# Kernel optimization log

Hardware: AMD Instinct MI355X
Metric: run time of the kernel (lower is better)

Reference implementation:

```python
import jax, jax.numpy as jnp
import numpy as np

HID = 64        # HID_DIM of seq2seq encoder
NL = 2          # N_LAYERS
D = HID * NL    # dim_hidden = 128
TYPES = 16      # node op types; Input=0, Const=1
MAX_ET = 32     # max edge_type id
NUM_ROUNDS = 2


def _gru_cell(x, h, Wih, Whh, bih, bhh):
    # torch GRU gate ordering: r, z, n
    gi = x @ Wih.T + bih
    gh = h @ Whh.T + bhh
    ir, iz, inn = jnp.split(gi, 3, axis=-1)
    hr, hz, hn = jnp.split(gh, 3, axis=-1)
    r = jax.nn.sigmoid(ir + hr)
    z = jax.nn.sigmoid(iz + hz)
    n = jnp.tanh(inn + r * hn)
    return (1.0 - z) * n + z * h


def _posenc(n, d):
    pos = jnp.arange(n, dtype=jnp.float32)[:, None]
    i = jnp.arange(d // 2, dtype=jnp.float32)[None, :]
    inv = jnp.exp(-jnp.log(10000.0) * (2.0 * i / d))
    pe = jnp.zeros((n, d), jnp.float32)
    pe = pe.at[:, 0::2].set(jnp.sin(pos * inv))
    pe = pe.at[:, 1::2].set(jnp.cos(pos * inv))
    return pe


def _forward(x, edge_index, edge_type, sim_res, seq_len,
             enc_Wih0, enc_Whh0, enc_bih0, enc_bhh0,
             enc_Wih1, enc_Whh1, enc_bih1, enc_bhh1,
             Wq, Wk, Wv, op_emb, mlp_W1, mlp_b1, mlp_W2, mlp_b2,
             gru_Wih, gru_Whh, gru_bih, gru_bhh):
    N = x.shape[0]
    # --- seq2seq encode (2-layer GRU over time), computed for all nodes then masked ---
    xs = jnp.swapaxes(sim_res[:, :seq_len, :], 0, 1)  # [T, N, W]
    h0 = jnp.zeros((N, HID), sim_res.dtype)
    h1 = jnp.zeros((N, HID), sim_res.dtype)

    def step(carry, xt):
        h0, h1 = carry
        h0 = _gru_cell(xt, h0, enc_Wih0, enc_Whh0, enc_bih0, enc_bhh0)
        h1 = _gru_cell(h0, h1, enc_Wih1, enc_Whh1, enc_bih1, enc_bhh1)
        return (h0, h1), None

    (h0, h1), _ = jax.lax.scan(step, (h0, h1), xs)
    enc = jnp.concatenate([h0, h1], axis=-1)  # [N, D] = permute(1,0,2).flatten(1)
    mask = (x[:, 0] == 1) | (x[:, 1] == 1)    # Input | Const nodes
    node_emb = jnp.where(mask[:, None], enc, 0.0)

    src, dst = edge_index[0], edge_index[1]
    edge_op = jnp.argmax(x[dst], axis=1)       # [E]
    pe = _posenc(MAX_ET, D)
    edge_feat = pe[edge_type] + op_emb[edge_op]  # [E, D]
    scale = 1.0 / jnp.sqrt(jnp.float32(D))

    for _ in range(NUM_ROUNDS):
        kf = node_emb[src] + edge_feat         # [E, D]
        q = node_emb[dst] @ Wq.T
        k = kf @ Wk.T
        v = kf @ Wv.T
        score = jnp.sum(q * k, axis=-1) * scale  # [E]
        m = jax.ops.segment_max(score, dst, num_segments=N)
        ex = jnp.exp(score - m[dst])
        den = jax.ops.segment_sum(ex, dst, num_segments=N)
        alpha = ex / (den[dst] + 1e-9)
        aggr = jax.ops.segment_sum(alpha[:, None] * v, dst, num_segments=N)  # [N, D]
        aggr = jax.nn.relu(aggr @ mlp_W1.T + mlp_b1) @ mlp_W2.T + mlp_b2
        node_emb = _gru_cell(aggr, node_emb, gru_Wih, gru_Whh, gru_bih, gru_bhh)
    return node_emb


def setup_inputs() -> dict:
    key = jax.random.key(0)
    ks = jax.random.split(key, 24)
    N, E, T, W = 20000, 320000, 32, 32
    s = 0.05

    def g(k, shape):
        return jax.random.normal(k, shape, dtype=jnp.float32) * s

    node_type = jax.random.randint(ks[0], (N,), 0, TYPES)
    x = jax.nn.one_hot(node_type, TYPES, dtype=jnp.float32)
    edge_index = jax.random.randint(ks[1], (2, E), 0, N)
    edge_type = jax.random.randint(ks[2], (E,), 0, MAX_ET)
    sim_res = jax.random.uniform(ks[3], (N, T, W), dtype=jnp.float32)
    return {
        "x": x, "edge_index": edge_index, "edge_type": edge_type,
        "sim_res": sim_res, "seq_len": 32,
        "enc_Wih0": g(ks[4], (3 * HID, W)), "enc_Whh0": g(ks[5], (3 * HID, HID)),
        "enc_bih0": g(ks[6], (3 * HID,)), "enc_bhh0": g(ks[7], (3 * HID,)),
        "enc_Wih1": g(ks[8], (3 * HID, HID)), "enc_Whh1": g(ks[9], (3 * HID, HID)),
        "enc_bih1": g(ks[10], (3 * HID,)), "enc_bhh1": g(ks[11], (3 * HID,)),
        "Wq": g(ks[12], (D, D)), "Wk": g(ks[13], (D, D)), "Wv": g(ks[14], (D, D)),
        "op_emb": g(ks[15], (TYPES, D)),
        "mlp_W1": g(ks[16], (D, D)), "mlp_b1": g(ks[17], (D,)),
        "mlp_W2": g(ks[18], (D, D)), "mlp_b2": g(ks[19], (D,)),
        "gru_Wih": g(ks[20], (3 * D, D)), "gru_Whh": g(ks[21], (3 * D, D)),
        "gru_bih": g(ks[22], (3 * D,)), "gru_bhh": g(ks[23], (3 * D,)),
    }


def reference(x, edge_index, edge_type, sim_res, seq_len,
              enc_Wih0, enc_Whh0, enc_bih0, enc_bhh0,
              enc_Wih1, enc_Whh1, enc_bih1, enc_bhh1,
              Wq, Wk, Wv, op_emb, mlp_W1, mlp_b1, mlp_W2, mlp_b2,
              gru_Wih, gru_Whh, gru_bih, gru_bhh):
    return _forward(x, edge_index, edge_type, sim_res, seq_len,
                    enc_Wih0, enc_Whh0, enc_bih0, enc_bhh0,
                    enc_Wih1, enc_Whh1, enc_bih1, enc_bhh1,
                    Wq, Wk, Wv, op_emb, mlp_W1, mlp_b1, mlp_W2, mlp_b2,
                    gru_Wih, gru_Whh, gru_bih, gru_bhh)
```

## Files before the change

### kernel.cpp

```cpp
#include <hip/hip_runtime.h>

typedef unsigned int uint;
typedef unsigned short ushort;

typedef __attribute__((ext_vector_type(8))) short bf8;
typedef __attribute__((ext_vector_type(4))) float f32x4;
typedef _Float16 half_t;
typedef __attribute__((ext_vector_type(8))) half_t h8;

__device__ __forceinline__ ushort f2bf(float f){
  uint u = __builtin_bit_cast(uint, f);
  u = u + 0x7FFFu + ((u >> 16) & 1u);
  return (ushort)(u >> 16);
}
__device__ __forceinline__ float bfl(uint u){ return __builtin_bit_cast(float, u << 16); }
__device__ __forceinline__ float bfh(uint u){ return __builtin_bit_cast(float, u & 0xFFFF0000u); }
__device__ __forceinline__ uint pkhalf(float a, float b){
  ushort lo = __builtin_bit_cast(ushort, (half_t)a);
  ushort hi = __builtin_bit_cast(ushort, (half_t)b);
  return (uint)lo | ((uint)hi << 16);
}
__device__ __forceinline__ float sigmoidf_(float x){ return 1.0f/(1.0f + __expf(-x)); }
__device__ __forceinline__ float tanhf_(float x){
  x = fminf(15.0f, fmaxf(-15.0f, x));
  float t = __expf(-2.0f*x);
  return (1.0f - t)/(1.0f + t);
}
__device__ __forceinline__ f32x4 mfma_f16(h8 a, h8 b, f32x4 c){
  return __builtin_amdgcn_mfma_f32_16x16x32_f16(a, b, c, 0, 0, 0);
}
__device__ __forceinline__ f32x4 mfma_bf(bf8 a, bf8 b, f32x4 c){
  return __builtin_amdgcn_mfma_f32_16x16x32_bf16(a, b, c, 0, 0, 0);
}
__device__ __forceinline__ h8 ldw8(const float* p){
  f32x4 a = *(const f32x4*)p, b = *(const f32x4*)(p+4);
  h8 v;
  #pragma unroll
  for (int j=0;j<4;j++){ v[j] = (half_t)a[j]; v[4+j] = (half_t)b[j]; }
  return v;
}

__global__ __launch_bounds__(256) void k_prep(const float* __restrict__ x,
    const int* __restrict__ dst,
    int* __restrict__ typ, int* __restrict__ mlist, int* __restrict__ cnt,
    int* __restrict__ deg, float* __restrict__ Hf, ushort* __restrict__ Hb,
    int N, int E){
  int i = blockIdx.x*256 + threadIdx.x;
  int total = gridDim.x*256;
  if (i < N){
    const float* xr = x + (size_t)i*16;
    int t = 0;
    #pragma unroll
    for (int j=0;j<16;j++) if (xr[j] > 0.5f) t = j;
    typ[i] = t;
    if (t < 2){
      int p = atomicAdd(cnt, 1);
      mlist[p] = i;
    }
  }
  if (i < E) atomicAdd(&deg[dst[i]], 1);
  f32x4 z4 = (f32x4)0.0f;
  for (int j = i; j < N*32; j += total) ((f32x4*)Hf)[j] = z4;
  uint2 z2; z2.x = 0u; z2.y = 0u;
  for (int j = i; j < N*32; j += total) ((uint2*)Hb)[j] = z2;
}

__global__ __launch_bounds__(256) void k_cvt(
    const float* wq, const float* wk, const float* wv,
    const float* w1, const float* w2, const float* wih, const float* whh,
    const float* __restrict__ op_emb,
    ushort* oqkv, ushort* o1, ushort* o2, ushort* oih, ushort* ohh,
    ushort* __restrict__ EF){
  int i = blockIdx.x*256 + threadIdx.x;
  int stride = gridDim.x*256;
  for (int j=i; j<16384; j+=stride){
    oqkv[j]       = f2bf(wq[j]);
    oqkv[16384+j] = f2bf(wk[j]);
    oqkv[32768+j] = f2bf(wv[j]);
    o1[j] = f2bf(w1[j]);
    o2[j] = f2bf(w2[j]);
  }
  for (int j=i; j<49152; j+=stride){ oih[j]=f2bf(wih[j]); ohh[j]=f2bf(whh[j]); }
  for (int idx=i; idx<512*128; idx+=stride){
    int r = idx >> 7, d = idx & 127;
    int et = r >> 4, op = r & 15;
    int j = d >> 1;
    float inv = __expf(-0.1439115683f * (float)j);
    float ang = (float)et * inv;
    float v = (d & 1) ? __cosf(ang) : __sinf(ang);
    EF[idx] = f2bf(v + op_emb[op*128 + d]);
  }
}

template<int RELU, int HASBIAS>
__global__ __launch_bounds__(256) void k_gemm(
    const ushort* __restrict__ A, const ushort* __restrict__ B,
    const float* __restrict__ bias, ushort* __restrict__ C, int M, int N){
  int lane = threadIdx.x & 63, wv = threadIdx.x >> 6;
  int tM = blockIdx.x*64 + (wv>>1)*32;
  int tN = blockIdx.y*64 + (wv&1)*32;
  int r16 = lane & 15, kg = (lane>>4)*8;
  f32x4 acc[2][2];
  #pragma unroll
  for (int i=0;i<2;i++)
    #pragma unroll
    for (int j=0;j<2;j++) acc[i][j] = (f32x4)0.0f;
  #pragma unroll
  for (int k0=0;k0<128;k0+=32){
    bf8 a[2], b[2];
    #pragma unroll
    for (int i=0;i<2;i++){
      int row = tM + i*16 + r16; if (row > M-1) row = M-1;
      a[i] = *(const bf8*)(A + (size_t)row*128 + k0 + kg);
    }
    #pragma unroll
    for (int j=0;j<2;j++){
      int col = tN + j*16 + r16;
      b[j] = *(const bf8*)(B + (size_t)col*128 + k0 + kg);
    }
    #pragma unroll
    for (int i=0;i<2;i++)
      #pragma unroll
      for (int j=0;j<2;j++)
        acc[i][j] = __builtin_amdgcn_mfma_f32_16x16x32_bf16(a[i], b[j], acc[i][j], 0, 0, 0);
  }
  #pragma unroll
  for (int i=0;i<2;i++)
    #pragma unroll
    for (int j=0;j<2;j++){
      int col = tN + j*16 + r16;
      float bs = HASBIAS ? bias[col] : 0.0f;
      #pragma unroll
      for (int q=0;q<4;q++){
        int row = tM + i*16 + (lane>>4)*4 + q;
        if (row < M){
          float v = acc[i][j][q] + bs;
          if (RELU) v = fmaxf(v, 0.0f);
          C[(size_t)row*N + col] = f2bf(v);
        }
      }
    }
}

__global__ __launch_bounds__(512, 1) void k_enc4(
    const float* __restrict__ sim_res, const int* __restrict__ seqlen,
    const float* __restrict__ Wih0, const float* __restrict__ Whh0,
    const float* __restrict__ bih0, const float* __restrict__ bhh0,
    const float* __restrict__ Wih1, const float* __restrict__ Whh1,
    const float* __restrict__ bih1, const float* __restrict__ bhh1,
    const int* __restrict__ mlist, const int* __restrict__ cntp,
    float* __restrict__ Hf, ushort* __restrict__ Hb){
  int C = *cntp;
  int base = blockIdx.x * 16;
  if (C == 0 || base >= C) return;
  int tid = threadIdx.x;
  int w = tid >> 6, l = tid & 63;
  int node = l & 15, hi = l >> 4;
  int grp = w >> 2;
  int ws  = w & 3;

  __shared__ int nod[16];
  __shared__ __align__(16) float  Xs[16*32*32];
  __shared__ __align__(16) ushort H0h[2][16*64], H1h[2][16*64];

  if (tid < 16){
    int idx = base + tid;
    nod[tid] = mlist[idx < C ? idx : C-1];
  }
  for (int i = tid; i < 16*64; i += 512){
    H0h[0][i] = 0; H0h[1][i] = 0; H1h[0][i] = 0; H1h[1][i] = 0;
  }
  __syncthreads();

  for (int m = tid; m < 4096; m += 512){
    int nm = m >> 8, tt = (m >> 3) & 31, c = m & 7;
    int cs = c ^ (nm & 7);
    f32x4 v = *(const f32x4*)(sim_res + (size_t)nod[nm]*1024 + tt*32 + cs*4);
    *(f32x4*)(Xs + m*4) = v;
  }

  int rr = 16*ws + node;
  h8 zf;
  #pragma unroll
  for (int j=0;j<8;j++) zf[j] = (half_t)0.f;
  h8 Ai_r[2] = {zf, zf}, Ai_z[2] = {zf, zf}, Ai_n[2] = {zf, zf};
  h8 Ah_r[2], Ah_z[2], Ah_n[2];
  if (grp == 0){
    Ai_r[0] = ldw8(Wih0 + (size_t)rr*32        + hi*8);
    Ai_z[0] = ldw8(Wih0 + (size_t)(64+rr)*32   + hi*8);
    Ai_n[0] = ldw8(Wih0 + (size_t)(128+rr)*32  + hi*8);
    #pragma unroll
    for (int s=0;s<2;s++){
      Ah_r[s] = ldw8(Whh0 + (size_t)rr*64       + s*32 + hi*8);
      Ah_z[s] = ldw8(Whh0 + (size_t)(64+rr)*64  + s*32 + hi*8);
      Ah_n[s] = ldw8(Whh0 + (size_t)(128+rr)*64 + s*32 + hi*8);
    }
  } else {
    #pragma unroll
    for (int s=0;s<2;s++){
      Ai_r[s] = ldw8(Wih1 + (size_t)rr*64       + s*32 + hi*8);
      Ai_z[s] = ldw8(Wih1 + (size_t)(64+rr)*64  + s*32 + hi*8);
      Ai_n[s] = ldw8(Wih1 + (size_t)(128+rr)*64 + s*32 + hi*8);
      Ah_r[s] = ldw8(Whh1 + (size_t)rr*64       + s*32 + hi*8);
      Ah_z[s] = ldw8(Whh1 + (size_t)(64+rr)*64  + s*32 + hi*8);
      Ah_n[s] = ldw8(Whh1 + (size_t)(128+rr)*64 + s*32 + hi*8);
    }
  }
  const float* bi = grp ? bih1 : bih0;
  const float* bh = grp ? bhh1 : bhh0;
  float br[4], bz[4], bni[4], bnh[4];
  #pragma unroll
  for (int q=0;q<4;q++){
    int row = 16*ws + hi*4 + q;
    br[q]  = bi[row]      + bh[row];
    bz[q]  = bi[64+row]   + bh[64+row];
    bni[q] = bi[128+row];
    bnh[q] = bh[128+row];
  }

  int T = *seqlen; if (T > 32) T = 32; if (T < 0) T = 0;
  float hm[4] = {0.f, 0.f, 0.f, 0.f};

  const int swz = (node & 7) << 4;
  const int wo  = node * 128;
  const int wba = 32*ws + 8*hi;
  const int rd0 = wo + ((16*hi) ^ swz);
  const int rd1 = wo + ((64 + 16*hi) ^ swz);
  const int xc0 = (2*hi)   ^ (node & 7);
  const int xc1 = (2*hi+1) ^ (node & 7);
  const float* xrow = Xs + node*1024;

  __syncthreads();

  for (int k = 0; k <= T; ++k){
    int cur = k & 1;
    bool act = grp ? (k >= 1) : (k < T);
    if (act){
      h8 in0 = zf, in1 = zf, st0, st1;
      if (grp == 0){
        f32x4 xa = *(const f32x4*)(xrow + k*32 + xc0*4);
        f32x4 xb = *(const f32x4*)(xrow + k*32 + xc1*4);
        #pragma unroll
        for (int j=0;j<4;j++){ in0[j] = (half_t)xa[j]; in0[4+j] = (half_t)xb[j]; }
        st0 = *(const h8*)((const char*)H0h[cur] + rd0);
        st1 = *(const h8*)((const char*)H0h[cur] + rd1);
      } else {
        in0 = *(const h8*)((const char*)H0h[cur] + rd0);
        in1 = *(const h8*)((const char*)H0h[cur] + rd1);
        st0 = *(const h8*)((const char*)H1h[cur] + rd0);
        st1 = *(const h8*)((const char*)H1h[cur] + rd1);
      }
      f32x4 ar = {br[0],br[1],br[2],br[3]};
      f32x4 az = {bz[0],bz[1],bz[2],bz[3]};
      f32x4 an = {bni[0],bni[1],bni[2],bni[3]};
      f32x4 hn = {bnh[0],bnh[1],bnh[2],bnh[3]};
      ar = mfma_f16(Ai_r[0], in0, ar);
      az = mfma_f16(Ai_z[0], in0, az);
      an = mfma_f16(Ai_n[0], in0, an);
      if (grp){
        ar = mfma_f16(Ai_r[1], in1, ar);
        az = mfma_f16(Ai_z[1], in1, az);
        an = mfma_f16(Ai_n[1], in1, an);
      }
      ar = mfma_f16(Ah_r[0], st0, ar); ar = mfma_f16(Ah_r[1], st1, ar);
      az = mfma_f16(Ah_z[0], st0, az); az = mfma_f16(Ah_z[1], st1, az);
      hn = mfma_f16(Ah_n[0], st0, hn); hn = mfma_f16(Ah_n[1], st1, hn);
      #pragma unroll
      for (int q=0;q<4;q++){
        float r = sigmoidf_(ar[q]);
        float z = sigmoidf_(az[q]);
        float n = tanhf_(an[q] + r*hn[q]);
        hm[q] = (1.f - z)*n + z*hm[q];
      }
      char* outb = grp ? (char*)H1h[cur^1] : (char*)H0h[cur^1];
      *(uint*)(outb + wo + ( wba      ^ swz)) = pkhalf(hm[0], hm[1]);
      *(uint*)(outb + wo + ((wba + 4) ^ swz)) = pkhalf(hm[2], hm[3]);
    }
    __syncthreads();
  }

  if (base + node < C){
    int nd = nod[node];
    int off = grp ? 64 : 0;
    #pragma unroll
    for (int q=0;q<4;q++){
      int j = off + 16*ws + hi*4 + q;
      Hf[(size_t)nd*128 + j] = hm[q];
      Hb[(size_t)nd*128 + j] = f2bf(hm[q]);
    }
  }
}

__global__ __launch_bounds__(1024) void k_scan(const int* __restrict__ deg,
    int* __restrict__ rowptr, int* __restrict__ cursor, int N){
  __shared__ int wsum[16];
  __shared__ int carry_s;
  int tid = threadIdx.x, lane = tid & 63, wid = tid >> 6;
  if (tid == 0) carry_s = 0;
  __syncthreads();
  int nch = (N + 1023) / 1024;
  for (int c=0; c<nch; ++c){
    int i = c*1024 + tid;
    int v = (i < N) ? deg[i] : 0;
    int x = v;
    #pragma unroll
    for (int off=1; off<64; off<<=1){
      int t = __shfl_up(x, off, 64);
      if (lane >= off) x += t;
    }
    if (lane == 63) wsum[wid] = x;
    __syncthreads();
    int base = carry_s;
    int woff = 0;
    for (int w2=0; w2<wid; ++w2) woff += wsum[w2];
    int excl = base + woff + x - v;
    if (i < N){ rowptr[i] = excl; cursor[i] = excl; }
    __syncthreads();
    if (tid == 0){
      int s = 0;
      for (int w2=0; w2<16; ++w2) s += wsum[w2];
      carry_s = base + s;
    }
    __syncthreads();
  }
  if (tid == 0) rowptr[N] = carry_s;
}

__global__ __launch_bounds__(256) void k_scatter(const int* __restrict__ src,
    const int* __restrict__ dst, const int* __restrict__ etype, const int* __restrict__ typ,
    int* __restrict__ cursor, int* __restrict__ es_src, int* __restrict__ es_tab, int E){
  int e = blockIdx.x*256 + threadIdx.x;
  if (e < E){
    int d = dst[e];
    int pos = atomicAdd(&cursor[d], 1);
    es_src[pos] = src[e];
    es_tab[pos] = etype[e]*16 + typ[d];
  }
}

__global__ __launch_bounds__(256) void k_attn(
    const uint* __restrict__ QKV, const uint* __restrict__ KVT,
    const int* __restrict__ rowptr, const int* __restrict__ es_src, const int* __restrict__ es_tab,
    uint* __restrict__ aggr, int N){
  int w = threadIdx.x >> 6, lane = threadIdx.x & 63;
  int dst = blockIdx.x*4 + w;
  if (dst >= N) return;
  uint qu = QKV[(size_t)dst*192 + lane];
  const float scale = 0.08838834764831845f;
  float q0 = bfl(qu)*scale, q1 = bfh(qu)*scale;
  int s0 = rowptr[dst], s1 = rowptr[dst+1];
  float m = -1e30f, den = 0.f, a0 = 0.f, a1 = 0.f;
  int p = s0;
  for (; p + 4 <= s1; p += 4){
    int se[4], te[4];
    #pragma unroll
    for (int e=0;e<4;e++){ se[e] = es_src[p+e]; te[e] = es_tab[p+e]; }
    uint ku[4], kt[4], vu[4], vt[4];
    #pragma unroll
    for (int e=0;e<4;e++){
      ku[e] = QKV[(size_t)se[e]*192 + 64 + lane];
      kt[e] = KVT[(size_t)te[e]*128 + lane];
      vu[e] = QKV[(size_t)se[e]*192 + 128 + lane];
      vt[e] = KVT[(size_t)te[e]*128 + 64 + lane];
    }
    float s[4];
    #pragma unroll
    for (int e=0;e<4;e++)
      s[e] = q0*(bfl(ku[e])+bfl(kt[e])) + q1*(bfh(ku[e])+bfh(kt[e]));
    #pragma unroll
    for (int off=32; off; off>>=1){
      #pragma unroll
      for (int e=0;e<4;e++) s[e] += __shfl_xor(s[e], off);
    }
    float nm = fmaxf(fmaxf(m, fmaxf(s[0], s[1])), fmaxf(s[2], s[3]));
    float c  = __expf(m - nm);
    float pw[4];
    #pragma unroll
    for (int e=0;e<4;e++) pw[e] = __expf(s[e] - nm);
    den = den*c + pw[0] + pw[1] + pw[2] + pw[3];
    a0 = a0*c; a1 = a1*c;
    #pragma unroll
    for (int e=0;e<4;e++){
      a0 += pw[e]*(bfl(vu[e])+bfl(vt[e]));
      a1 += pw[e]*(bfh(vu[e])+bfh(vt[e]));
    }
    m = nm;
  }
  for (; p < s1; ++p){
    int src = es_src[p], tb = es_tab[p];
    uint ku = QKV[(size_t)src*192 + 64 + lane],  kt = KVT[(size_t)tb*128 + lane];
    uint vu = QKV[(size_t)src*192 + 128 + lane], vt = KVT[(size_t)tb*128 + 64 + lane];
    float s = q0*(bfl(ku)+bfl(kt)) + q1*(bfh(ku)+bfh(kt));
    #pragma unroll
    for (int off=32; off; off>>=1) s += __shfl_xor(s, off);
    float nm = fmaxf(m, s);
    float c  = __expf(m - nm);
    float pw = __expf(s - nm);
    den = den*c + pw;
    a0  = a0*c + pw*(bfl(vu)+bfl(vt));
    a1  = a1*c + pw*(bfh(vu)+bfh(vt));
    m = nm;
  }
  float inv = 1.0f/(den + 1e-9f);
  a0 *= inv; a1 *= inv;
  aggr[(size_t)dst*64 + lane] = ((uint)f2bf(a1) << 16) | (uint)f2bf(a0);
}

__global__ __launch_bounds__(512, 2) void k_fused(
    const ushort* __restrict__ Ag,
    const ushort* __restrict__ W1b, const float* __restrict__ b1,
    const ushort* __restrict__ W2b, const float* __restrict__ b2,
    const ushort* __restrict__ Wih, const ushort* __restrict__ Whh,
    const float* __restrict__ bih, const float* __restrict__ bhh,
    const ushort* Hbf, const float* Hf_in,
    float* Hf_out, ushort* Hb_out, int M){
  int lane = threadIdx.x & 63, w = threadIdx.x >> 6;
  int nb = blockIdx.x * 32;
  int r16 = lane & 15, kq = lane >> 4;
  const int col = w*16 + r16;

  __shared__ __align__(16) ushort T[32*128];

  bf8 agld[2][4], ahld[2][4];
  #pragma unroll
  for (int i=0;i<2;i++){
    int grow = nb + i*16 + r16; if (grow > M-1) grow = M-1;
    #pragma unroll
    for (int ks=0;ks<4;ks++){
      agld[i][ks] = *(const bf8*)(Ag  + (size_t)grow*128 + ks*32 + kq*8);
      ahld[i][ks] = *(const bf8*)(Hbf + (size_t)grow*128 + ks*32 + kq*8);
    }
  }
  float hprev[2][4];
  #pragma unroll
  for (int i=0;i<2;i++)
    #pragma unroll
    for (int q=0;q<4;q++){
      int node = nb + i*16 + kq*4 + q;
      hprev[i][q] = Hf_in[(size_t)(node < M ? node : M-1)*128 + col];
    }

  {
    f32x4 a0 = (f32x4)0.0f, a1v = (f32x4)0.0f;
    #pragma unroll
    for (int ks=0; ks<4; ++ks){
      bf8 wb = *(const bf8*)(W1b + (size_t)col*128 + ks*32 + kq*8);
      a0  = mfma_bf(agld[0][ks], wb, a0);
      a1v = mfma_bf(agld[1][ks], wb, a1v);
    }
    float bs = b1[col];
    #pragma unroll
    for (int q=0;q<4;q++){
      int row0 = kq*4 + q, row1 = 16 + kq*4 + q;
      *(ushort*)((char*)T + ((row0*256 + col*2) ^ ((row0&7)<<4))) = f2bf(fmaxf(a0[q]  + bs, 0.0f));
      *(ushort*)((char*)T + ((row1*256 + col*2) ^ ((row1&7)<<4))) = f2bf(fmaxf(a1v[q] + bs, 0.0f));
    }
  }
  __syncthreads();

  {
    f32x4 a0 = (f32x4)0.0f, a1v = (f32x4)0.0f;
    #pragma unroll
    for (int ks=0; ks<4; ++ks){
      bf8 wb = *(const bf8*)(W2b + (size_t)col*128 + ks*32 + kq*8);
      bf8 ax0, ax1;
      {
        int row = r16;
        ax0 = *(const bf8*)((const char*)T + row*256 + ((ks*64 + kq*16) ^ ((row&7)<<4)));
      }
      {
        int row = 16 + r16;
        ax1 = *(const bf8*)((const char*)T + row*256 + ((ks*64 + kq*16) ^ ((row&7)<<4)));
      }
      a0  = mfma_bf(ax0, wb, a0);
      a1v = mfma_bf(ax1, wb, a1v);
    }
    __syncthreads();
    float bs = b2[col];
    #pragma unroll
    for (int q=0;q<4;q++){
      int row0 = kq*4 + q, row1 = 16 + kq*4 + q;
      *(ushort*)((char*)T + ((row0*256 + col*2) ^ ((row0&7)<<4))) = f2bf(a0[q]  + bs);
      *(ushort*)((char*)T + ((row1*256 + col*2) ^ ((row1&7)<<4))) = f2bf(a1v[q] + bs);
    }
  }
  __syncthreads();

  f32x4 ar[2], az[2], ani[2], anh[2];
  #pragma unroll
  for (int i=0;i<2;i++){
    ar[i] = (f32x4)0.0f; az[i] = (f32x4)0.0f;
    ani[i] = (f32x4)0.0f; anh[i] = (f32x4)0.0f;
  }
  #pragma unroll
  for (int ks=0; ks<4; ++ks){
    int off = ks*32 + kq*8;
    bf8 wri = *(const bf8*)(Wih + (size_t)col*128       + off);
    bf8 wrh = *(const bf8*)(Whh + (size_t)col*128       + off);
    bf8 wzi = *(const bf8*)(Wih + (size_t)(128+col)*128 + off);
    bf8 wzh = *(const bf8*)(Whh + (size_t)(128+col)*128 + off);
    bf8 wni = *(const bf8*)(Wih + (size_t)(256+col)*128 + off);
    bf8 wnh = *(const bf8*)(Whh + (size_t)(256+col)*128 + off);
    bf8 ax0, ax1;
    {
      int row = r16;
      ax0 = *(const bf8*)((const char*)T + row*256 + ((ks*64 + kq*16) ^ ((row&7)<<4)));
    }
    {
      int row = 16 + r16;
      ax1 = *(const bf8*)((const char*)T + row*256 + ((ks*64 + kq*16) ^ ((row&7)<<4)));
    }
    ar[0]  = mfma_bf(ax0,         wri, ar[0]);
    ar[0]  = mfma_bf(ahld[0][ks], wrh, ar[0]);
    az[0]  = mfma_bf(ax0,         wzi, az[0]);
    az[0]  = mfma_bf(ahld[0][ks], wzh, az[0]);
    ani[0] = mfma_bf(ax0,         wni, ani[0]);
    anh[0] = mfma_bf(ahld[0][ks], wnh, anh[0]);
    ar[1]  = mfma_bf(ax1,         wri, ar[1]);
    ar[1]  = mfma_bf(ahld[1][ks], wrh, ar[1]);
    az[1]  = mfma_bf(ax1,         wzi, az[1]);
    az[1]  = mfma_bf(ahld[1][ks], wzh, az[1]);
    ani[1] = mfma_bf(ax1,         wni, ani[1]);
    anh[1] = mfma_bf(ahld[1][ks], wnh, anh[1]);
  }
  float br_  = bih[col]     + bhh[col];
  float bz_  = bih[128+col] + bhh[128+col];
  float bni_ = bih[256+col];
  float bnh_ = bhh[256+col];
  #pragma unroll
  for (int i=0;i<2;i++)
    #pragma unroll
    for (int q=0;q<4;q++){
      int node = nb + i*16 + kq*4 + q;
      if (node < M){
        float r = sigmoidf_(ar[i][q] + br_);
        float z = sigmoidf_(az[i][q] + bz_);
        float n = tanhf_(ani[i][q] + bni_ + r*(anh[i][q] + bnh_));
        float h = hprev[i][q];
        float o = (1.f - z)*n + z*h;
        Hf_out[(size_t)node*128 + col] = o;
        Hb_out[(size_t)node*128 + col] = f2bf(o);
      }
    }
}

extern "C" void kernel_launch(void* const* d_in, const int* in_sizes, int n_in,
                              void* d_out, int out_size, void* d_ws, size_t ws_size,
                              hipStream_t stream){
  const float* x       = (const float*)d_in[0];
  const int*   ei      = (const int*)d_in[1];
  const int*   etype   = (const int*)d_in[2];
  const float* sim_res = (const float*)d_in[3];
  const int*   seqlen  = (const int*)d_in[4];
  const float* eWih0 = (const float*)d_in[5];
  const float* eWhh0 = (const float*)d_in[6];
  const float* ebih0 = (const float*)d_in[7];
  const float* ebhh0 = (const float*)d_in[8];
  const float* eWih1 = (const float*)d_in[9];
  const float* eWhh1 = (const float*)d_in[10];
  const float* ebih1 = (const float*)d_in[11];
  const float* ebhh1 = (const float*)d_in[12];
  const float* Wq = (const float*)d_in[13];
  const float* Wk = (const float*)d_in[14];
  const float* Wv = (const float*)d_in[15];
  const float* op_emb = (const float*)d_in[16];
  const float* W1 = (const float*)d_in[17];
  const float* b1 = (const float*)d_in[18];
  const float* W2 = (const float*)d_in[19];
  const float* b2 = (const float*)d_in[20];
  const float* gWih = (const float*)d_in[21];
  const float* gWhh = (const float*)d_in[22];
  const float* gbih = (const float*)d_in[23];
  const float* gbhh = (const float*)d_in[24];

  const int N = in_sizes[0] / 16;
  const int E = in_sizes[2];

  char* p = (char*)d_ws;
  auto take = [&](size_t b)->void*{ void* r = (void*)p; p += (b + 255) & ~(size_t)255; return r; };

  float*  Hf    = (float*) take((size_t)N*128*4);
  ushort* Hb    = (ushort*)take((size_t)N*128*2);
  ushort* QKV   = (ushort*)take((size_t)N*384*2);
  ushort* Ag    = (ushort*)take((size_t)N*128*2);
  ushort* EF    = (ushort*)take((size_t)512*128*2);
  ushort* KVtab = (ushort*)take((size_t)512*256*2);
  ushort* wqkv  = (ushort*)take((size_t)3*16384*2);
  ushort* w1_b  = (ushort*)take((size_t)16384*2);
  ushort* w2_b  = (ushort*)take((size_t)16384*2);
  ushort* wih_b = (ushort*)take((size_t)49152*2);
  ushort* whh_b = (ushort*)take((size_t)49152*2);
  int* typ    = (int*)take((size_t)N*4);
  int* mlist  = (int*)take((size_t)N*4);
  int* cnt    = (int*)take(256);
  int* deg    = (int*)take((size_t)N*4);
  int* rowptr = (int*)take((size_t)(N+1)*4);
  int* cursor = (int*)take((size_t)N*4);
  int* es_src = (int*)take((size_t)E*4);
  int* es_tab = (int*)take((size_t)E*4);

  hipMemsetAsync(cnt, 0, 4, stream);
  hipMemsetAsync(deg, 0, (size_t)N*4, stream);

  int gE = (E + 255) / 256;
  k_prep<<<gE, 256, 0, stream>>>(x, ei + E, typ, mlist, cnt, deg, Hf, Hb, N, E);
  k_cvt<<<256, 256, 0, stream>>>(Wq, Wk, Wv, W1, W2, gWih, gWhh, op_emb,
                                 wqkv, w1_b, w2_b, wih_b, whh_b, EF);
  k_gemm<0,0><<<dim3(8,4), 256, 0, stream>>>(EF, wqkv + 16384, nullptr, KVtab, 512, 256);
  k_enc4<<<(N+15)/16, 512, 0, stream>>>(sim_res, seqlen, eWih0, eWhh0, ebih0, ebhh0,
                                        eWih1, eWhh1, ebih1, ebhh1, mlist, cnt, Hf, Hb);
  k_scan<<<1, 1024, 0, stream>>>(deg, rowptr, cursor, N);
  k_scatter<<<gE, 256, 0, stream>>>(ei, ei + E, etype, typ, cursor, es_src, es_tab, E);

  dim3 gq((N+63)/64, 6);
  for (int r=0; r<2; ++r){
    k_gemm<0,0><<<gq, 256, 0, stream>>>(Hb, wqkv, nullptr, QKV, N, 384);
    k_attn<<<(N+3)/4, 256, 0, stream>>>((const uint*)QKV, (const uint*)KVtab,
                                        rowptr, es_src, es_tab, (uint*)Ag, N);
    float* hf_out = (r == 1) ? (float*)d_out : Hf;
    k_fused<<<(N+31)/32, 512, 0, stream>>>(Ag, w1_b, b1, w2_b, b2,
                                           wih_b, whh_b, gbih, gbhh,
                                           Hb, Hf, hf_out, Hb, N);
  }
}
```

Baseline: 309.0 us.

## Split edge attention into score pass and aggregation pass; blocked single-pass scan

The fused online-softmax attention kernel is split in two. The first kernel computes the edge scores, stores them along with per-node max and inverse denominator, and the second reloads each score and gathers V with no rescaling. Separately, the degree scan now has each thread sum a contiguous chunk, so a single block pass replaces the chunked loop with repeated barriers. The split adds a kernel launch and a score round-trip through memory per round, in exchange for shorter dependency chains in each pass.

```diff
diff --git a/kernel.cpp b/kernel.cpp
--- a/kernel.cpp
+++ b/kernel.cpp
@@ -294,36 +294,27 @@
 __global__ __launch_bounds__(1024) void k_scan(const int* __restrict__ deg,
     int* __restrict__ rowptr, int* __restrict__ cursor, int N){
   __shared__ int wsum[16];
-  __shared__ int carry_s;
   int tid = threadIdx.x, lane = tid & 63, wid = tid >> 6;
-  if (tid == 0) carry_s = 0;
+  int CH = (N + 1023) >> 10;
+  int start = tid * CH;
+  int local = 0;
+  for (int j=0;j<CH;j++){ int i = start+j; if (i < N) local += deg[i]; }
+  int x = local;
+  #pragma unroll
+  for (int off=1; off<64; off<<=1){
+    int t = __shfl_up(x, off, 64);
+    if (lane >= off) x += t;
+  }
+  if (lane == 63) wsum[wid] = x;
   __syncthreads();
-  int nch = (N + 1023) / 1024;
-  for (int c=0; c<nch; ++c){
-    int i = c*1024 + tid;
-    int v = (i < N) ? deg[i] : 0;
-    int x = v;
-    #pragma unroll
-    for (int off=1; off<64; off<<=1){
-      int t = __shfl_up(x, off, 64);
-      if (lane >= off) x += t;
-    }
-    if (lane == 63) wsum[wid] = x;
-    __syncthreads();
-    int base = carry_s;
-    int woff = 0;
-    for (int w2=0; w2<wid; ++w2) woff += wsum[w2];
-    int excl = base + woff + x - v;
-    if (i < N){ rowptr[i] = excl; cursor[i] = excl; }
-    __syncthreads();
-    if (tid == 0){
-      int s = 0;
-      for (int w2=0; w2<16; ++w2) s += wsum[w2];
-      carry_s = base + s;
-    }
-    __syncthreads();
-  }
-  if (tid == 0) rowptr[N] = carry_s;
+  int woff = 0;
+  for (int w2=0; w2<wid; ++w2) woff += wsum[w2];
+  int run = woff + x - local;
+  for (int j=0;j<CH;j++){
+    int i = start+j;
+    if (i < N){ rowptr[i] = run; cursor[i] = run; run += deg[i]; }
+  }
+  if (tid == 1023) rowptr[N] = run;
 }
 
 __global__ __launch_bounds__(256) void k_scatter(const int* __restrict__ src,
@@ -338,10 +329,10 @@
   }
 }
 
-__global__ __launch_bounds__(256) void k_attn(
+__global__ __launch_bounds__(256) void k_attn1(
     const uint* __restrict__ QKV, const uint* __restrict__ KVT,
     const int* __restrict__ rowptr, const int* __restrict__ es_src, const int* __restrict__ es_tab,
-    uint* __restrict__ aggr, int N){
+    float* __restrict__ score, float* __restrict__ mden, int N){
   int w = threadIdx.x >> 6, lane = threadIdx.x & 63;
   int dst = blockIdx.x*4 + w;
   if (dst >= N) return;
@@ -349,60 +340,80 @@
   const float scale = 0.08838834764831845f;
   float q0 = bfl(qu)*scale, q1 = bfh(qu)*scale;
   int s0 = rowptr[dst], s1 = rowptr[dst+1];
-  float m = -1e30f, den = 0.f, a0 = 0.f, a1 = 0.f;
+  float m = -1e30f, den = 0.f;
+  int p = s0;
+  for (; p + 2 <= s1; p += 2){
+    int srcA = es_src[p],   tbA = es_tab[p];
+    int srcB = es_src[p+1], tbB = es_tab[p+1];
+    uint kuA = QKV[(size_t)srcA*192 + 64 + lane], ktA = KVT[(size_t)tbA*128 + lane];
+    uint kuB = QKV[(size_t)srcB*192 + 64 + lane], ktB = KVT[(size_t)tbB*128 + lane];
+    float sA = q0*(bfl(kuA)+bfl(ktA)) + q1*(bfh(kuA)+bfh(ktA));
+    float sB = q0*(bfl(kuB)+bfl(ktB)) + q1*(bfh(kuB)+bfh(ktB));
+    #pragma unroll
+    for (int off=32; off; off>>=1){
+      sA += __shfl_xor(sA, off);
+      sB += __shfl_xor(sB, off);
+    }
+    if (lane == 0){ score[p] = sA; score[p+1] = sB; }
+    float nm = fmaxf(m, fmaxf(sA, sB));
+    float c  = __expf(m - nm);
+    den = den*c + __expf(sA - nm) + __expf(sB - nm);
+    m = nm;
+  }
+  for (; p < s1; ++p){
+    int src = es_src[p], tb = es_tab[p];
+    uint ku = QKV[(size_t)src*192 + 64 + lane], kt = KVT[(size_t)tb*128 + lane];
+    float s = q0*(bfl(ku)+bfl(kt)) + q1*(bfh(ku)+bfh(kt));
+    #pragma unroll
+    for (int off=32; off; off>>=1) s += __shfl_xor(s, off);
+    if (lane == 0) score[p] = s;
+    float nm = fmaxf(m, s);
+    den = den*__expf(m - nm) + __expf(s - nm);
+    m = nm;
+  }
+  if (lane == 0){
+    mden[dst]     = m;
+    mden[N + dst] = 1.0f/(den + 1e-9f);
+  }
+}
+
+__global__ __launch_bounds__(256) void k_attn2(
+    const uint* __restrict__ QKV, const uint* __restrict__ KVT,
+    const int* __restrict__ rowptr, const int* __restrict__ es_src, const int* __restrict__ es_tab,
+    const float* __restrict__ score, const float* __restrict__ mden,
+    uint* __restrict__ aggr, int N){
+  int w = threadIdx.x >> 6, lane = threadIdx.x & 63;
+  int dst = blockIdx.x*4 + w;
+  if (dst >= N) return;
+  float m   = mden[dst];
+  float inv = mden[N + dst];
+  int s0 = rowptr[dst], s1 = rowptr[dst+1];
+  float a0 = 0.f, a1 = 0.f;
   int p = s0;
   for (; p + 4 <= s1; p += 4){
-    int se[4], te[4];
-    #pragma unroll
-    for (int e=0;e<4;e++){ se[e] = es_src[p+e]; te[e] = es_tab[p+e]; }
-    uint ku[4], kt[4], vu[4], vt[4];
+    float al[4];
+    uint vu[4], vt[4];
     #pragma unroll
     for (int e=0;e<4;e++){
-      ku[e] = QKV[(size_t)se[e]*192 + 64 + lane];
-      kt[e] = KVT[(size_t)te[e]*128 + lane];
-      vu[e] = QKV[(size_t)se[e]*192 + 128 + lane];
-      vt[e] = KVT[(size_t)te[e]*128 + 64 + lane];
-    }
-    float s[4];
-    #pragma unroll
-    for (int e=0;e<4;e++)
-      s[e] = q0*(bfl(ku[e])+bfl(kt[e])) + q1*(bfh(ku[e])+bfh(kt[e]));
-    #pragma unroll
-    for (int off=32; off; off>>=1){
-      #pragma unroll
-      for (int e=0;e<4;e++) s[e] += __shfl_xor(s[e], off);
-    }
-    float nm = fmaxf(fmaxf(m, fmaxf(s[0], s[1])), fmaxf(s[2], s[3]));
-    float c  = __expf(m - nm);
-    float pw[4];
-    #pragma unroll
-    for (int e=0;e<4;e++) pw[e] = __expf(s[e] - nm);
-    den = den*c + pw[0] + pw[1] + pw[2] + pw[3];
-    a0 = a0*c; a1 = a1*c;
+      int src = es_src[p+e], tb = es_tab[p+e];
+      al[e] = __expf(score[p+e] - m) * inv;
+      vu[e] = QKV[(size_t)src*192 + 128 + lane];
+      vt[e] = KVT[(size_t)tb*128 + 64 + lane];
+    }
     #pragma unroll
     for (int e=0;e<4;e++){
-      a0 += pw[e]*(bfl(vu[e])+bfl(vt[e]));
-      a1 += pw[e]*(bfh(vu[e])+bfh(vt[e]));
-    }
-    m = nm;
+      a0 += al[e]*(bfl(vu[e])+bfl(vt[e]));
+      a1 += al[e]*(bfh(vu[e])+bfh(vt[e]));
+    }
   }
   for (; p < s1; ++p){
     int src = es_src[p], tb = es_tab[p];
-    uint ku = QKV[(size_t)src*192 + 64 + lane],  kt = KVT[(size_t)tb*128 + lane];
-    uint vu = QKV[(size_t)src*192 + 128 + lane], vt = KVT[(size_t)tb*128 + 64 + lane];
-    float s = q0*(bfl(ku)+bfl(kt)) + q1*(bfh(ku)+bfh(kt));
-    #pragma unroll
-    for (int off=32; off; off>>=1) s += __shfl_xor(s, off);
-    float nm = fmaxf(m, s);
-    float c  = __expf(m - nm);
-    float pw = __expf(s - nm);
-    den = den*c + pw;
-    a0  = a0*c + pw*(bfl(vu)+bfl(vt));
-    a1  = a1*c + pw*(bfh(vu)+bfh(vt));
-    m = nm;
-  }
-  float inv = 1.0f/(den + 1e-9f);
-  a0 *= inv; a1 *= inv;
+    float al = __expf(score[p] - m) * inv;
+    uint vu = QKV[(size_t)src*192 + 128 + lane];
+    uint vt = KVT[(size_t)tb*128 + 64 + lane];
+    a0 += al*(bfl(vu)+bfl(vt));
+    a1 += al*(bfh(vu)+bfh(vt));
+  }
   aggr[(size_t)dst*64 + lane] = ((uint)f2bf(a1) << 16) | (uint)f2bf(a0);
 }
 
@@ -590,6 +601,8 @@
   ushort* w2_b  = (ushort*)take((size_t)16384*2);
   ushort* wih_b = (ushort*)take((size_t)49152*2);
   ushort* whh_b = (ushort*)take((size_t)49152*2);
+  float* score = (float*)take((size_t)E*4);
+  float* mden  = (float*)take((size_t)2*N*4);
   int* typ    = (int*)take((size_t)N*4);
   int* mlist  = (int*)take((size_t)N*4);
   int* cnt    = (int*)take(256);
@@ -615,8 +628,11 @@
   dim3 gq((N+63)/64, 6);
   for (int r=0; r<2; ++r){
     k_gemm<0,0><<<gq, 256, 0, stream>>>(Hb, wqkv, nullptr, QKV, N, 384);
-    k_attn<<<(N+3)/4, 256, 0, stream>>>((const uint*)QKV, (const uint*)KVtab,
-                                        rowptr, es_src, es_tab, (uint*)Ag, N);
+    k_attn1<<<(N+3)/4, 256, 0, stream>>>((const uint*)QKV, (const uint*)KVtab,
+                                         rowptr, es_src, es_tab, score, mden, N);
+    k_attn2<<<(N+3)/4, 256, 0, stream>>>((const uint*)QKV, (const uint*)KVtab,
+                                         rowptr, es_src, es_tab, score, mden,
+                                         (uint*)Ag, N);
     float* hf_out = (r == 1) ? (float*)d_out : Hf;
     k_fused<<<(N+31)/32, 512, 0, stream>>>(Ag, w1_b, b1, w2_b, b2,
                                            wih_b, whh_b, gbih, gbhh,
```

New measurement: 367.2 us. 1.19x slower.
